# Performance work log

Hardware: AMD Instinct MI355X
Metric: run time of the kernel (lower is better)

Reference implementation:

```python
import jax, jax.numpy as jnp
import numpy as np

CONF_THRES = 0.8
NMS_THRES = 0.4
MAX_DET = 300          # fixed capacity for jit-compatible NMS output
N_BOXES = 262144
N_CLASSES = 80


def xywh2xyxy(x):
    xy, wh = x[..., :2], x[..., 2:4]
    return jnp.concatenate([xy - wh * 0.5, xy + wh * 0.5], axis=-1)


def bbox_iou(box, boxes):
    # one box [4] vs many [N,4]; original uses the +1 pixel-area convention
    x1 = jnp.maximum(box[0], boxes[:, 0])
    y1 = jnp.maximum(box[1], boxes[:, 1])
    x2 = jnp.minimum(box[2], boxes[:, 2])
    y2 = jnp.minimum(box[3], boxes[:, 3])
    inter = jnp.clip(x2 - x1 + 1, 0) * jnp.clip(y2 - y1 + 1, 0)
    a1 = (box[2] - box[0] + 1) * (box[3] - box[1] + 1)
    a2 = (boxes[:, 2] - boxes[:, 0] + 1) * (boxes[:, 3] - boxes[:, 1] + 1)
    return inter / (a1 + a2 - inter + 1e-16)


def nms_single(pred):
    # pred: [N, 85] raw YOLO output for one image
    boxes = xywh2xyxy(pred[:, :4])
    obj = pred[:, 4]
    cls_scores = pred[:, 5:]
    class_conf = cls_scores.max(axis=-1)
    class_pred = jnp.argmax(cls_scores, axis=-1).astype(pred.dtype)
    valid = obj >= CONF_THRES
    score = obj * class_conf
    # sort valid boxes by descending score; invalid pushed to the end
    order = jnp.argsort(jnp.where(valid, -score, jnp.inf))
    det = jnp.concatenate(
        [boxes, obj[:, None], class_conf[:, None], class_pred[:, None]], axis=1
    )[order]  # [N, 7] = x1,y1,x2,y2,obj,class_conf,class_pred
    valid = valid[order]

    def step(valid, _):
        idx = jnp.argmax(valid)            # first still-valid (= highest score)
        any_valid = jnp.any(valid)
        cur = det[idx]
        iou = bbox_iou(cur[:4], det[:, :4])
        invalid = (iou > NMS_THRES) & (det[:, 6] == cur[6]) & valid
        # weighted box merge over the suppressed group (as in original NMS)
        w = jnp.where(invalid, det[:, 4], 0.0)
        merged = (w[:, None] * det[:, :4]).sum(0) / (w.sum() + 1e-16)
        out = jnp.where(any_valid,
                        jnp.concatenate([merged, cur[4:]]),
                        jnp.zeros(7, pred.dtype))
        return valid & ~invalid, (out, any_valid)

    _, (kept, kept_valid) = jax.lax.scan(step, valid, None, length=MAX_DET)
    return kept, kept_valid  # [MAX_DET,7], [MAX_DET]


def setup_inputs() -> dict:
    key = jax.random.key(0)
    detections = jax.random.uniform(key, (1, N_BOXES, 5 + N_CLASSES), dtype=jnp.float32)
    return {"detections": detections}


def reference(detections):
    kept, kv = nms_single(detections[0])
    d = kept[:, 5:]                        # [MAX_DET, 2] = (class_conf, class_pred)
    conf_key = jnp.where(kv, d[:, 0], -jnp.inf)  # padded rows sort to the end
    order = jnp.argsort(conf_key)          # ascending (torch argsort)
    d = d[order][::-1]                     # torch.flip -> descending class_conf
    kv = kv[order][::-1]
    probs = jnp.where(kv, d[:, 0], 0.0)    # self.probs
    ids = d[:, 1][None, :]                 # self.ids, shape [1, MAX_DET]
    return ids, probs
```

## Files before the change

### kernel.cpp

```cpp
#include <hip/hip_runtime.h>

#pragma clang fp contract(off)

#define NBOX 262144
#define NCLS 80
#define ROWS 85
#define CAP 1024
#define NSUB 8
#define SUBCAP 128
#define POOL 8192
#define BPT 2
#define S1BOX 512

typedef unsigned long long ull;

__global__ __launch_bounds__(1024) void k_init(int* __restrict__ cnt_pad,
                                               int* __restrict__ pool_count,
                                               int* __restrict__ done_count) {
    const int t = threadIdx.x;
    for (int i = t; i < NCLS * NSUB * 16; i += 1024) cnt_pad[i] = 0;
    if (t == 0) { *pool_count = 0; *done_count = 0; }
}

__global__ __launch_bounds__(256) void k_stage1(const float* __restrict__ det,
                                                int* __restrict__ cnt_pad,
                                                ull* __restrict__ key2,
                                                float* __restrict__ conf2,
                                                float4* __restrict__ box2) {
    __shared__ int s_wl[S1BOX];
    __shared__ float s_obj[S1BOX];
    __shared__ int s_nv;
    const int t = threadIdx.x;
    const int b0 = blockIdx.x * S1BOX;
    const int sb = blockIdx.x & (NSUB - 1);

    if (t == 0) s_nv = 0;
    __syncthreads();

    float obj[BPT];
    #pragma unroll
    for (int i = 0; i < BPT; i++)
        obj[i] = det[(size_t)(b0 + (i << 8) + t) * ROWS + 4];
    #pragma unroll
    for (int i = 0; i < BPT; i++) {
        if (obj[i] >= 0.8f) {
            int r = atomicAdd(&s_nv, 1);
            s_wl[r] = (i << 8) + t;
            s_obj[r] = obj[i];
        }
    }
    __syncthreads();
    const int nv = s_nv;

    const int grp = t >> 4, c = t & 15;
    const int lane = t & 63;
    #pragma unroll 2
    for (int r0 = 0; r0 < nv; r0 += 16) {
        int widx = r0 + grp;
        if (widx < nv) {
            int b = s_wl[widx];
            const float* p = det + (size_t)(b0 + b) * ROWS;
            float aux = (c < 5) ? p[c] : 0.0f;
            float v0 = p[5 + c];
            float v1 = p[21 + c];
            float v2 = p[37 + c];
            float v3 = p[53 + c];
            float v4 = p[69 + c];
            float mv = v0; int mj = c;
            if (v1 > mv) { mv = v1; mj = 16 + c; }
            if (v2 > mv) { mv = v2; mj = 32 + c; }
            if (v3 > mv) { mv = v3; mj = 48 + c; }
            if (v4 > mv) { mv = v4; mj = 64 + c; }
            #pragma unroll
            for (int off = 8; off; off >>= 1) {
                float ov = __shfl_xor(mv, off);
                int oj = __shfl_xor(mj, off);
                if (ov > mv || (ov == mv && oj < mj)) { mv = ov; mj = oj; }
            }
            int gb = lane & 48;
            float x = __shfl(aux, gb + 0);
            float y = __shfl(aux, gb + 1);
            float w = __shfl(aux, gb + 2);
            float h = __shfl(aux, gb + 3);
            if (c == 0) {
                float ob = s_obj[widx];
                float score = ob * mv;
                float hw = w * 0.5f, hh = h * 0.5f;
                int gi = b0 + b;
                int r = atomicAdd(&cnt_pad[((mj * NSUB + sb) << 4)], 1);
                if (r < SUBCAP) {
                    int pos = (mj << 10) + (sb << 7) + r;
                    key2[pos] = ((ull)(~__float_as_uint(score)) << 32) | (unsigned)gi;
                    conf2[pos] = mv;
                    box2[pos] = make_float4(x - hw, y - hh, x + hw, y + hh);
                }
            }
        }
    }
}

template <int L>
__device__ __forceinline__ int exact_alive(ull (&k)[L]) {
    int a = 0;
    #pragma unroll
    for (int j = 0; j < L; j++) a += (int)__popcll(__ballot(k[j] != ~0ULL));
    return a;
}

template <int L>
__device__ __forceinline__ void pick_loop(ull (&k)[L], float4 (&bx)[L], float (&cf)[L],
                                          float (&ar)[L],
                                          int lane, int& alive, int& np,
                                          ull* pkey, float* pconf, int stopAt) {
    while (alive > stopAt && np < 300) {
        ull v[L]; int ix[L];
        #pragma unroll
        for (int j = 0; j < L; j++) { v[j] = k[j]; ix[j] = j; }
        #pragma unroll
        for (int s = L >> 1; s; s >>= 1) {
            #pragma unroll
            for (int j = 0; j < s; j++)
                if (v[j + s] < v[j]) { v[j] = v[j + s]; ix[j] = ix[j + s]; }
        }
        ull lm = v[0]; const int lj = ix[0];
        float4 cb = bx[0]; float cc = cf[0];
        #pragma unroll
        for (int j = 1; j < L; j++) if (j == lj) { cb = bx[j]; cc = cf[j]; }
        unsigned lo = (unsigned)lm;
        unsigned hi = (unsigned)(lm >> 32);
        unsigned mh = hi;
        #pragma unroll
        for (int off = 32; off; off >>= 1) {
            unsigned o = __shfl_xor(mh, off);
            mh = o < mh ? o : mh;
        }
        ull wb = __ballot(hi == mh);
        ull gm; int wl2;
        if (mh == 0xFFFFFFFFu || __popcll(wb) != 1) {
            ull g = (hi == mh) ? lm : ~0ULL;
            #pragma unroll
            for (int off = 32; off; off >>= 1) {
                ull o = __shfl_xor(g, off);
                if (o < g) g = o;
            }
            gm = g;
            if (gm == ~0ULL) { alive = 0; break; }
            wb = __ballot(lm == gm);
            wl2 = (int)__ffsll((long long)wb) - 1;
        } else {
            wl2 = (int)__ffsll((long long)wb) - 1;
            gm = ((ull)mh << 32) | (ull)__shfl(lo, wl2);
        }
        cb.x = __shfl(cb.x, wl2); cb.y = __shfl(cb.y, wl2);
        cb.z = __shfl(cb.z, wl2); cb.w = __shfl(cb.w, wl2);
        cc = __shfl(cc, wl2);
        if (lane == 0) { pkey[np] = gm; pconf[np] = cc; }
        np++;
        float a1 = (cb.z - cb.x + 1.0f) * (cb.w - cb.y + 1.0f);
        #pragma unroll
        for (int j = 0; j < L; j++) {
            if (k[j] != ~0ULL) {
                float4 b = bx[j];
                float xx1 = fmaxf(cb.x, b.x), yy1 = fmaxf(cb.y, b.y);
                float xx2 = fminf(cb.z, b.z), yy2 = fminf(cb.w, b.w);
                float iw = xx2 - xx1 + 1.0f, ih = yy2 - yy1 + 1.0f;
                float inter = fmaxf(iw, 0.0f) * fmaxf(ih, 0.0f);
                float iou = inter / (a1 + ar[j] - inter + 1e-16f);
                if (iou > 0.4f) k[j] = ~0ULL;
            }
        }
        if ((np & 7) == 0) alive = exact_alive(k);
    }
}

__device__ __forceinline__ void compact16to4(ull (&k)[16], float4 (&bx)[16], float (&cf)[16],
                                             ull (&k2)[4], float4 (&b2)[4], float (&c2)[4],
                                             float (&a2)[4],
                                             int lane, int alive,
                                             ull* dk, float4* db, float* dc) {
    int ci = 0;
    #pragma unroll
    for (int j = 0; j < 16; j++) if (k[j] != ~0ULL) ci++;
    int inc = ci;
    for (int off = 1; off < 64; off <<= 1) {
        int o = __shfl_up(inc, off);
        if (lane >= off) inc += o;
    }
    int wp = inc - ci;
    #pragma unroll
    for (int j = 0; j < 16; j++)
        if (k[j] != ~0ULL) { dk[wp] = k[j]; db[wp] = bx[j]; dc[wp] = cf[j]; wp++; }
    #pragma unroll
    for (int j = 0; j < 4; j++) {
        int pos = lane + (j << 6);
        bool ok = pos < alive;
        k2[j] = ok ? dk[pos] : ~0ULL;
        b2[j] = ok ? db[pos] : make_float4(0.f, 0.f, 0.f, 0.f);
        c2[j] = ok ? dc[pos] : 0.0f;
        a2[j] = (b2[j].z - b2[j].x + 1.0f) * (b2[j].w - b2[j].y + 1.0f);
    }
}

__device__ __forceinline__ void bsort512(ull (&x)[8], int lane) {
    #pragma unroll
    for (int k = 2; k <= 512; k <<= 1) {
        #pragma unroll
        for (int j = k >> 1; j >= 64; j >>= 1) {
            const int jr = j >> 6;
            #pragma unroll
            for (int r2 = 0; r2 < 8; r2++) {
                if ((r2 & jr) == 0) {
                    const bool asc = (((r2 << 6) & k) == 0);
                    ull a = x[r2], b = x[r2 | jr];
                    if ((a > b) == asc) { x[r2] = b; x[r2 | jr] = a; }
                }
            }
        }
        #pragma unroll
        for (int j = ((k >> 1) > 32 ? 32 : (k >> 1)); j >= 1; j >>= 1) {
            #pragma unroll
            for (int r2 = 0; r2 < 8; r2++) {
                int i = (r2 << 6) + lane;
                bool asc = ((i & k) == 0);
                ull o = __shfl_xor(x[r2], j);
                bool lower = ((lane & j) == 0);
                ull mn = x[r2] < o ? x[r2] : o;
                ull mx2 = x[r2] < o ? o : x[r2];
                x[r2] = (asc == lower) ? mn : mx2;
            }
        }
    }
}

__global__ __launch_bounds__(256) void k_nmsfinal(const int* __restrict__ cnt_pad,
                                                  const ull* __restrict__ key2,
                                                  const float* __restrict__ conf2,
                                                  const float4* __restrict__ box2,
                                                  ull* __restrict__ pool_key,
                                                  float* __restrict__ pool_conf,
                                                  int* __restrict__ pool_cls,
                                                  int* __restrict__ pool_count,
                                                  int* __restrict__ done_count,
                                                  float* __restrict__ out) {
    __shared__ ull sk[256];
    __shared__ float4 sbx[256];
    __shared__ float scf[256];
    __shared__ ull pkey[304];
    __shared__ float pconf[304];
    __shared__ int s_fin;
    __shared__ int s_hist[256];
    __shared__ int s_wt[4];
    __shared__ int s_stat[4];
    __shared__ ull s_buf[512];
    __shared__ unsigned s_cb[512];
    __shared__ unsigned s_cl[512];

    const int c = blockIdx.x, t = threadIdx.x, lane = t & 63, wave = t >> 6;

    if (wave == 0) {
        const int s0 = c << 10;
        ull k16[16]; float4 b16[16]; float c16[16]; float a16[16];
        #pragma unroll
        for (int j = 0; j < 16; j++) {
            int pos = lane + (j << 6);
            k16[j] = key2[s0 + pos];
            b16[j] = box2[s0 + pos];
            c16[j] = conf2[s0 + pos];
        }
        int cv0 = 0;
        if (lane < NSUB) cv0 = min(cnt_pad[((c * NSUB + lane) << 4)], SUBCAP);
        int ntot = cv0;
        #pragma unroll
        for (int off = 32; off; off >>= 1) ntot += __shfl_xor(ntot, off);
        #pragma unroll
        for (int j = 0; j < 16; j++) {
            int pos = lane + (j << 6);
            int lim = __shfl(cv0, pos >> 7);
            bool ok = (pos & (SUBCAP - 1)) < lim;
            if (!ok) {
                k16[j] = ~0ULL;
                b16[j] = make_float4(0.f, 0.f, 0.f, 0.f);
                c16[j] = 0.0f;
            }
            a16[j] = (b16[j].z - b16[j].x + 1.0f) * (b16[j].w - b16[j].y + 1.0f);
        }
        int alive = ntot, np = 0;
        pick_loop<16>(k16, b16, c16, a16, lane, alive, np, pkey, pconf, 256);
        if (np < 300) {
            alive = exact_alive(k16);
            if (alive > 0) {
                ull k4[4]; float4 b4[4]; float c4[4]; float a4[4];
                compact16to4(k16, b16, c16, k4, b4, c4, a4, lane, alive, sk, sbx, scf);
                pick_loop<4>(k4, b4, c4, a4, lane, alive, np, pkey, pconf, 0);
            }
        }

        int npw = min(np, 300);
        int base = 0;
        if (lane == 0 && npw) base = atomicAdd(pool_count, npw);
        base = __shfl(base, 0);
        for (int j = lane; j < npw; j += 64) {
            int pp = base + j;
            if (pp < POOL) {
                ull gm = pkey[j];
                ull pk = ((ull)((unsigned)(gm >> 32) & 0x7FFFFFFFu) << 32)
                       | ((gm & 0xFFFFFFFFull) << 14) | (ull)pp;
                __hip_atomic_store(&pool_key[pp], pk,
                                   __ATOMIC_RELAXED, __HIP_MEMORY_SCOPE_AGENT);
                __hip_atomic_store(&pool_conf[pp], pconf[j],
                                   __ATOMIC_RELAXED, __HIP_MEMORY_SCOPE_AGENT);
                __hip_atomic_store(&pool_cls[pp], c,
                                   __ATOMIC_RELAXED, __HIP_MEMORY_SCOPE_AGENT);
            }
        }
        asm volatile("s_waitcnt vmcnt(0)" ::: "memory");
    }
    __syncthreads();
    if (t == 0) {
        int ticket = atomicAdd(done_count, 1);
        s_fin = (ticket == NCLS - 1) ? 1 : 0;
    }
    __syncthreads();
    if (!s_fin) return;

    const int K = min(__hip_atomic_load(pool_count, __ATOMIC_RELAXED,
                                        __HIP_MEMORY_SCOPE_AGENT), POOL);
    ull key[32];
    #pragma unroll
    for (int j = 0; j < 32; j++) {
        int pos = t + (j << 8);
        key[j] = (pos < K) ? __hip_atomic_load(&pool_key[pos], __ATOMIC_RELAXED,
                                               __HIP_MEMORY_SCOPE_AGENT)
                           : ~0ULL;
    }

    const bool selAll = (K <= 511);
    int sh = 55;
    ull pfin = 0;
    if (!selAll) {
        ull p = 0;
        int gBelow = 0, r = 300;
        while (true) {
            s_hist[t] = 0;
            __syncthreads();
            #pragma unroll
            for (int j = 0; j < 32; j++) {
                ull kk = key[j];
                if ((kk >> (sh + 8)) == p)
                    atomicAdd(&s_hist[(int)((kk >> sh) & 0xFFull)], 1);
            }
            __syncthreads();
            int v = s_hist[t];
            int incv = v;
            for (int off = 1; off < 64; off <<= 1) {
                int o = __shfl_up(incv, off);
                if (lane >= off) incv += o;
            }
            if (lane == 63) s_wt[wave] = incv;
            __syncthreads();
            int wo = 0;
            #pragma unroll
            for (int w2 = 0; w2 < 4; w2++) if (w2 < wave) wo += s_wt[w2];
            int cumIncl = wo + incv;
            int cumExcl = cumIncl - v;
            if (cumExcl < r && r <= cumIncl) {
                s_stat[0] = t; s_stat[1] = cumExcl; s_stat[2] = cumIncl;
            }
            __syncthreads();
            int D = s_stat[0], below = s_stat[1], incl = s_stat[2];
            if (gBelow + incl <= 511 || sh == 7) {
                pfin = (p << 8) | (ull)D;
                break;
            }
            p = (p << 8) | (ull)D;
            gBelow += below;
            r = 300 - gBelow;
            sh -= 8;
            __syncthreads();
        }
    }

    if (t == 0) s_stat[3] = 0;
    __syncthreads();
    int ci = 0;
    #pragma unroll
    for (int j = 0; j < 32; j++) {
        ull kk = key[j];
        bool sel = selAll ? ((kk >> 63) == 0) : ((kk >> sh) <= pfin);
        if (sel) ci++;
    }
    int inc = ci;
    for (int off = 1; off < 64; off <<= 1) {
        int o = __shfl_up(inc, off);
        if (lane >= off) inc += o;
    }
    int wtot = __shfl(inc, 63);
    int wbase2 = 0;
    if (lane == 0 && wtot) wbase2 = atomicAdd(&s_stat[3], wtot);
    wbase2 = __shfl(wbase2, 0);
    int wp = wbase2 + inc - ci;
    #pragma unroll
    for (int j = 0; j < 32; j++) {
        ull kk = key[j];
        bool sel = selAll ? ((kk >> 63) == 0) : ((kk >> sh) <= pfin);
        if (sel) s_buf[wp++] = kk;
    }
    __syncthreads();
    const int S = s_stat[3];
    for (int i = t; i < 512; i += 256) if (i >= S) s_buf[i] = ~0ULL;
    __syncthreads();
    if (wave != 0) return;

    #pragma clang loop unroll(disable)
    for (int pass = 0; pass < 2; pass++) {
        ull x[8];
        #pragma unroll
        for (int r2 = 0; r2 < 8; r2++) x[r2] = s_buf[(r2 << 6) + lane];
        bsort512(x, lane);
        if (pass == 0) {
            #pragma unroll
            for (int r2 = 0; r2 < 8; r2++) {
                int i = (r2 << 6) + lane;
                ull kk = x[r2];
                ull k2 = ~0ULL;
                if (i < 300 && kk != ~0ULL) {
                    int pidx = (int)(kk & 0x3FFFull);
                    unsigned cb = __float_as_uint(
                        __hip_atomic_load(&pool_conf[pidx], __ATOMIC_RELAXED,
                                          __HIP_MEMORY_SCOPE_AGENT));
                    unsigned cl = (unsigned)__hip_atomic_load(&pool_cls[pidx],
                                          __ATOMIC_RELAXED, __HIP_MEMORY_SCOPE_AGENT);
                    s_cb[i] = cb; s_cl[i] = cl;
                    k2 = ((ull)(~cb) << 32) | (unsigned)(~i);
                }
                s_buf[i] = k2;
            }
        } else {
            #pragma unroll
            for (int r2 = 0; r2 < 8; r2++) {
                int i = (r2 << 6) + lane;
                if (i < 300) {
                    ull kk = x[r2];
                    float idv = 0.0f, pv = 0.0f;
                    if (kk != ~0ULL) {
                        int slot = (int)(~(unsigned)(kk & 0xFFFFFFFFull));
                        pv = __uint_as_float(s_cb[slot]);
                        idv = (float)(int)s_cl[slot];
                    }
                    out[i] = idv;
                    out[300 + i] = pv;
                }
            }
        }
    }
}

extern "C" void kernel_launch(void* const* d_in, const int* in_sizes, int n_in,
                              void* d_out, int out_size, void* d_ws, size_t ws_size,
                              hipStream_t stream) {
    const float* det = (const float*)d_in[0];
    float* out = (float*)d_out;
    char* ws = (char*)d_ws;

    int* cnt_pad = (int*)(ws + 0);
    int* pool_count = (int*)(ws + 40960);
    int* done_count = (int*)(ws + 40964);
    ull* key2 = (ull*)(ws + 41024);
    float* conf2 = (float*)(ws + 696384);
    float4* box2 = (float4*)(ws + 1024064);
    ull* pool_key = (ull*)(ws + 2334784);
    float* pool_conf = (float*)(ws + 2400320);
    int* pool_cls = (int*)(ws + 2433088);

    k_init<<<1, 1024, 0, stream>>>(cnt_pad, pool_count, done_count);
    k_stage1<<<NBOX / S1BOX, 256, 0, stream>>>(det, cnt_pad, key2, conf2, box2);
    k_nmsfinal<<<NCLS, 256, 0, stream>>>(cnt_pad, key2, conf2, box2,
                                         pool_key, pool_conf, pool_cls, pool_count,
                                         done_count, out);
}
```

Baseline: 179.1 us.

## Stage per-class candidates in shared memory SoA and drop the 16-to-4 compaction

The whole block now cooperatively loads the 1024 candidate keys, boxes, confidences and areas into shared memory as structure-of-arrays. Wave 0 keeps only the keys in registers and reads box coordinates from LDS during IoU suppression. This replaces the two-phase register pick loop with its compaction step. The aim is to cut register pressure and the load latency on the single active wave, at the cost of LDS reads on every suppression pass and the loss of the cheaper 4-per-lane tail phase.

```diff
diff --git a/kernel.cpp b/kernel.cpp
--- a/kernel.cpp
+++ b/kernel.cpp
@@ -99,106 +99,11 @@
     }
 }
 
-template <int L>
-__device__ __forceinline__ int exact_alive(ull (&k)[L]) {
+__device__ __forceinline__ int exact_alive16(ull (&k)[16]) {
     int a = 0;
     #pragma unroll
-    for (int j = 0; j < L; j++) a += (int)__popcll(__ballot(k[j] != ~0ULL));
+    for (int j = 0; j < 16; j++) a += (int)__popcll(__ballot(k[j] != ~0ULL));
     return a;
-}
-
-template <int L>
-__device__ __forceinline__ void pick_loop(ull (&k)[L], float4 (&bx)[L], float (&cf)[L],
-                                          float (&ar)[L],
-                                          int lane, int& alive, int& np,
-                                          ull* pkey, float* pconf, int stopAt) {
-    while (alive > stopAt && np < 300) {
-        ull v[L]; int ix[L];
-        #pragma unroll
-        for (int j = 0; j < L; j++) { v[j] = k[j]; ix[j] = j; }
-        #pragma unroll
-        for (int s = L >> 1; s; s >>= 1) {
-            #pragma unroll
-            for (int j = 0; j < s; j++)
-                if (v[j + s] < v[j]) { v[j] = v[j + s]; ix[j] = ix[j + s]; }
-        }
-        ull lm = v[0]; const int lj = ix[0];
-        float4 cb = bx[0]; float cc = cf[0];
-        #pragma unroll
-        for (int j = 1; j < L; j++) if (j == lj) { cb = bx[j]; cc = cf[j]; }
-        unsigned lo = (unsigned)lm;
-        unsigned hi = (unsigned)(lm >> 32);
-        unsigned mh = hi;
-        #pragma unroll
-        for (int off = 32; off; off >>= 1) {
-            unsigned o = __shfl_xor(mh, off);
-            mh = o < mh ? o : mh;
-        }
-        ull wb = __ballot(hi == mh);
-        ull gm; int wl2;
-        if (mh == 0xFFFFFFFFu || __popcll(wb) != 1) {
-            ull g = (hi == mh) ? lm : ~0ULL;
-            #pragma unroll
-            for (int off = 32; off; off >>= 1) {
-                ull o = __shfl_xor(g, off);
-                if (o < g) g = o;
-            }
-            gm = g;
-            if (gm == ~0ULL) { alive = 0; break; }
-            wb = __ballot(lm == gm);
-            wl2 = (int)__ffsll((long long)wb) - 1;
-        } else {
-            wl2 = (int)__ffsll((long long)wb) - 1;
-            gm = ((ull)mh << 32) | (ull)__shfl(lo, wl2);
-        }
-        cb.x = __shfl(cb.x, wl2); cb.y = __shfl(cb.y, wl2);
-        cb.z = __shfl(cb.z, wl2); cb.w = __shfl(cb.w, wl2);
-        cc = __shfl(cc, wl2);
-        if (lane == 0) { pkey[np] = gm; pconf[np] = cc; }
-        np++;
-        float a1 = (cb.z - cb.x + 1.0f) * (cb.w - cb.y + 1.0f);
-        #pragma unroll
-        for (int j = 0; j < L; j++) {
-            if (k[j] != ~0ULL) {
-                float4 b = bx[j];
-                float xx1 = fmaxf(cb.x, b.x), yy1 = fmaxf(cb.y, b.y);
-                float xx2 = fminf(cb.z, b.z), yy2 = fminf(cb.w, b.w);
-                float iw = xx2 - xx1 + 1.0f, ih = yy2 - yy1 + 1.0f;
-                float inter = fmaxf(iw, 0.0f) * fmaxf(ih, 0.0f);
-                float iou = inter / (a1 + ar[j] - inter + 1e-16f);
-                if (iou > 0.4f) k[j] = ~0ULL;
-            }
-        }
-        if ((np & 7) == 0) alive = exact_alive(k);
-    }
-}
-
-__device__ __forceinline__ void compact16to4(ull (&k)[16], float4 (&bx)[16], float (&cf)[16],
-                                             ull (&k2)[4], float4 (&b2)[4], float (&c2)[4],
-                                             float (&a2)[4],
-                                             int lane, int alive,
-                                             ull* dk, float4* db, float* dc) {
-    int ci = 0;
-    #pragma unroll
-    for (int j = 0; j < 16; j++) if (k[j] != ~0ULL) ci++;
-    int inc = ci;
-    for (int off = 1; off < 64; off <<= 1) {
-        int o = __shfl_up(inc, off);
-        if (lane >= off) inc += o;
-    }
-    int wp = inc - ci;
-    #pragma unroll
-    for (int j = 0; j < 16; j++)
-        if (k[j] != ~0ULL) { dk[wp] = k[j]; db[wp] = bx[j]; dc[wp] = cf[j]; wp++; }
-    #pragma unroll
-    for (int j = 0; j < 4; j++) {
-        int pos = lane + (j << 6);
-        bool ok = pos < alive;
-        k2[j] = ok ? dk[pos] : ~0ULL;
-        b2[j] = ok ? db[pos] : make_float4(0.f, 0.f, 0.f, 0.f);
-        c2[j] = ok ? dc[pos] : 0.0f;
-        a2[j] = (b2[j].z - b2[j].x + 1.0f) * (b2[j].w - b2[j].y + 1.0f);
-    }
 }
 
 __device__ __forceinline__ void bsort512(ull (&x)[8], int lane) {
@@ -242,9 +147,10 @@
                                                   int* __restrict__ pool_count,
                                                   int* __restrict__ done_count,
                                                   float* __restrict__ out) {
-    __shared__ ull sk[256];
-    __shared__ float4 sbx[256];
-    __shared__ float scf[256];
+    __shared__ float s_x1[CAP], s_y1[CAP], s_x2[CAP], s_y2[CAP];
+    __shared__ float s_area[CAP], s_conf[CAP];
+    __shared__ ull s_key[CAP];
+    __shared__ int s_cnt[NSUB];
     __shared__ ull pkey[304];
     __shared__ float pconf[304];
     __shared__ int s_fin;
@@ -256,43 +162,103 @@
     __shared__ unsigned s_cl[512];
 
     const int c = blockIdx.x, t = threadIdx.x, lane = t & 63, wave = t >> 6;
+    const int s0 = c << 10;
+
+    ull rk[4]; float4 rb[4]; float rc[4];
+    #pragma unroll
+    for (int i = 0; i < 4; i++) {
+        int pos = t + (i << 8);
+        rk[i] = key2[s0 + pos];
+        rb[i] = box2[s0 + pos];
+        rc[i] = conf2[s0 + pos];
+    }
+    if (t < NSUB) s_cnt[t] = min(cnt_pad[((c * NSUB + t) << 4)], SUBCAP);
+    __syncthreads();
+    #pragma unroll
+    for (int i = 0; i < 4; i++) {
+        int pos = t + (i << 8);
+        bool ok = (pos & (SUBCAP - 1)) < s_cnt[pos >> 7];
+        float4 b = ok ? rb[i] : make_float4(0.f, 0.f, 0.f, 0.f);
+        s_key[pos] = ok ? rk[i] : ~0ULL;
+        s_x1[pos] = b.x; s_y1[pos] = b.y; s_x2[pos] = b.z; s_y2[pos] = b.w;
+        s_area[pos] = (b.z - b.x + 1.0f) * (b.w - b.y + 1.0f);
+        s_conf[pos] = ok ? rc[i] : 0.0f;
+    }
+    __syncthreads();
 
     if (wave == 0) {
-        const int s0 = c << 10;
-        ull k16[16]; float4 b16[16]; float c16[16]; float a16[16];
-        #pragma unroll
-        for (int j = 0; j < 16; j++) {
-            int pos = lane + (j << 6);
-            k16[j] = key2[s0 + pos];
-            b16[j] = box2[s0 + pos];
-            c16[j] = conf2[s0 + pos];
-        }
         int cv0 = 0;
-        if (lane < NSUB) cv0 = min(cnt_pad[((c * NSUB + lane) << 4)], SUBCAP);
+        if (lane < NSUB) cv0 = s_cnt[lane];
         int ntot = cv0;
         #pragma unroll
         for (int off = 32; off; off >>= 1) ntot += __shfl_xor(ntot, off);
+
+        ull k16[16];
         #pragma unroll
-        for (int j = 0; j < 16; j++) {
-            int pos = lane + (j << 6);
-            int lim = __shfl(cv0, pos >> 7);
-            bool ok = (pos & (SUBCAP - 1)) < lim;
-            if (!ok) {
-                k16[j] = ~0ULL;
-                b16[j] = make_float4(0.f, 0.f, 0.f, 0.f);
-                c16[j] = 0.0f;
-            }
-            a16[j] = (b16[j].z - b16[j].x + 1.0f) * (b16[j].w - b16[j].y + 1.0f);
-        }
+        for (int j = 0; j < 16; j++) k16[j] = s_key[(j << 6) + lane];
+
         int alive = ntot, np = 0;
-        pick_loop<16>(k16, b16, c16, a16, lane, alive, np, pkey, pconf, 256);
-        if (np < 300) {
-            alive = exact_alive(k16);
-            if (alive > 0) {
-                ull k4[4]; float4 b4[4]; float c4[4]; float a4[4];
-                compact16to4(k16, b16, c16, k4, b4, c4, a4, lane, alive, sk, sbx, scf);
-                pick_loop<4>(k4, b4, c4, a4, lane, alive, np, pkey, pconf, 0);
-            }
+        while (alive > 0 && np < 300) {
+            ull v8[8]; int i8[8];
+            #pragma unroll
+            for (int j = 0; j < 8; j++) {
+                bool l = k16[j + 8] < k16[j];
+                v8[j] = l ? k16[j + 8] : k16[j];
+                i8[j] = l ? j + 8 : j;
+            }
+            #pragma unroll
+            for (int j = 0; j < 4; j++) {
+                if (v8[j + 4] < v8[j]) { v8[j] = v8[j + 4]; i8[j] = i8[j + 4]; }
+            }
+            if (v8[2] < v8[0]) { v8[0] = v8[2]; i8[0] = i8[2]; }
+            if (v8[3] < v8[1]) { v8[1] = v8[3]; i8[1] = i8[3]; }
+            if (v8[1] < v8[0]) { v8[0] = v8[1]; i8[0] = i8[1]; }
+            ull lm = v8[0]; const int lj = i8[0];
+
+            unsigned lo = (unsigned)lm;
+            unsigned hi = (unsigned)(lm >> 32);
+            unsigned mh = hi;
+            #pragma unroll
+            for (int off = 32; off; off >>= 1) {
+                unsigned o = __shfl_xor(mh, off);
+                mh = o < mh ? o : mh;
+            }
+            ull wb = __ballot(hi == mh);
+            ull gm; int wl2;
+            if (mh == 0xFFFFFFFFu || __popcll(wb) != 1) {
+                ull g = (hi == mh) ? lm : ~0ULL;
+                #pragma unroll
+                for (int off = 32; off; off >>= 1) {
+                    ull o = __shfl_xor(g, off);
+                    if (o < g) g = o;
+                }
+                gm = g;
+                if (gm == ~0ULL) { alive = 0; break; }
+                wb = __ballot(lm == gm);
+                wl2 = (int)__ffsll((long long)wb) - 1;
+            } else {
+                wl2 = (int)__ffsll((long long)wb) - 1;
+                gm = ((ull)mh << 32) | (ull)__shfl(lo, wl2);
+            }
+            int wpos = __shfl((lj << 6) + lane, wl2);
+            float cx1 = s_x1[wpos], cy1 = s_y1[wpos];
+            float cx2 = s_x2[wpos], cy2 = s_y2[wpos];
+            float a1 = s_area[wpos];
+            if (lane == 0) { pkey[np] = gm; pconf[np] = s_conf[wpos]; }
+            np++;
+            #pragma unroll
+            for (int j = 0; j < 16; j++) {
+                if (k16[j] != ~0ULL) {
+                    int pos = (j << 6) + lane;
+                    float xx1 = fmaxf(cx1, s_x1[pos]), yy1 = fmaxf(cy1, s_y1[pos]);
+                    float xx2 = fminf(cx2, s_x2[pos]), yy2 = fminf(cy2, s_y2[pos]);
+                    float iw = xx2 - xx1 + 1.0f, ih = yy2 - yy1 + 1.0f;
+                    float inter = fmaxf(iw, 0.0f) * fmaxf(ih, 0.0f);
+                    float iou = inter / (a1 + s_area[pos] - inter + 1e-16f);
+                    if (iou > 0.4f) k16[j] = ~0ULL;
+                }
+            }
+            if ((np & 7) == 0) alive = exact_alive16(k16);
         }
 
         int npw = min(np, 300);
```

New measurement: 178.2 us. About the same (-0.5%).
